# Kernel optimization log

Hardware: AMD Instinct MI355X
Metric: run time of the kernel (lower is better)

The kernel has to match this reference:

```python
import jax, jax.numpy as jnp
import numpy as np

N_QUBITS = 11   # state dim 2**11 = 2048
N_LAYERS = 6
BATCH = 8192


def _rz(phi):
    # RZ(phi) = diag(e^{-i phi/2}, e^{+i phi/2}); phi scalar -> (2,2), phi (B,) -> (B,2,2)
    e = jnp.exp(-0.5j * phi.astype(jnp.complex64))
    z = jnp.zeros_like(e)
    return jnp.stack([jnp.stack([e, z], -1), jnp.stack([z, jnp.conj(e)], -1)], -2)


def _ry(theta):
    # RY(theta) = [[cos t, -sin t], [sin t, cos t]], t = theta/2
    t = 0.5 * theta.astype(jnp.float32)
    c = jnp.cos(t).astype(jnp.complex64)
    s = jnp.sin(t).astype(jnp.complex64)
    return jnp.stack([jnp.stack([c, -s], -1), jnp.stack([s, c], -1)], -2)


def _apply_1q(state, U, q, n):
    # state: (B, 2**n); qubit q is the q-th most-significant bit of the ket index
    B = state.shape[0]
    st = state.reshape(B, 2 ** q, 2, 2 ** (n - 1 - q))
    if U.ndim == 2:   # shared (trainable) gate
        st = jnp.einsum('ab,sxby->sxay', U, st)
    else:             # per-sample (data-encoding) gate, U: (B,2,2)
        st = jnp.einsum('sab,sxby->sxay', U, st)
    return st.reshape(B, 2 ** n)


def _apply_cnot(state, c, n):
    # CNOT with control c, target c+1 (adjacent in the chain)
    B = state.shape[0]
    st = state.reshape(B, 2 ** c, 2, 2, 2 ** (n - 2 - c))
    st = jnp.stack([st[:, :, 0], st[:, :, 1, ::-1]], axis=2)  # flip target when control=1
    return st.reshape(B, 2 ** n)


def _forward(X, params):
    n, L = N_QUBITS, N_LAYERS
    B = X.shape[0]
    # pad/truncate features to n_qubits (matches build_circuit)
    Xe = X[:, :n] if X.shape[1] >= n else jnp.pad(X, ((0, 0), (0, n - X.shape[1])))
    state = jnp.zeros((B, 2 ** n), jnp.complex64).at[:, 0].set(1.0)  # |0...0>
    for l in range(L):
        for q in range(n):
            state = _apply_1q(state, _rz(params[l, q, 0]), q, n)
            state = _apply_1q(state, _ry(params[l, q, 1]), q, n)
            state = _apply_1q(state, _rz(params[l, q, 2]), q, n)
            if l == L - 1:  # data re-upload RY only on the last layer (per source)
                state = _apply_1q(state, _ry(Xe[:, q]), q, n)
        if n > 1:
            for c in range(n - 1):
                state = _apply_cnot(state, c, n)
    return state  # (B, 2**n) complex64


def setup_inputs() -> dict:
    key = jax.random.key(0)
    k1, k2 = jax.random.split(key)
    X = jax.random.uniform(k1, (BATCH, N_QUBITS), jnp.float32) * (2.0 * np.pi)
    params = jax.random.normal(k2, (N_LAYERS, N_QUBITS, 3), jnp.float32) * 0.01
    return {"X": X, "params": params}


def reference(X, params):
    state = _forward(X, params)
    # return real/imag stacked so the output is a real float32 array
    return jnp.stack([state.real, state.imag], -1)  # (B, 2**n, 2)
```

## Files before the change

### kernel.cpp

```cpp
#include <hip/hip_runtime.h>
#include <math.h>

#define NQ   11
#define DIM  2048
#define NL   6

typedef float v2f __attribute__((ext_vector_type(2)));

__host__ __device__ constexpr int swzA(int x) {
    return x ^ ((x >> 6) & 31) ^ ((x & 2) << 3) ^ ((x & 1) << 3);
}
__host__ __device__ constexpr int swzB(int x) {
    return x ^ ((x >> 7) & 7) ^ ((x >> 3) & 14) ^ ((x >> 6) & 8);
}

__device__ __forceinline__ float2 cfma2(float2 u, float2 a, float2 v, float2 b) {
    float2 r;
    r.x = u.x*a.x - u.y*a.y + v.x*b.x - v.y*b.y;
    r.y = u.x*a.y + u.y*a.x + v.x*b.y + v.y*b.x;
    return r;
}

template<int CTRL>
__device__ __forceinline__ v2f dpp_xor(v2f v) {
    const int x = __builtin_amdgcn_update_dpp(
        0, __float_as_int(v.x), CTRL, 0xF, 0xF, true);
    const int y = __builtin_amdgcn_update_dpp(
        0, __float_as_int(v.y), CTRL, 0xF, 0xF, true);
    v2f r; r.x = __int_as_float(x); r.y = __int_as_float(y);
    return r;
}

__global__ __launch_bounds__(256) void qnn_shared_kernel(
    const float* __restrict__ P,
    float2* __restrict__ ws)
{
    __shared__ float2 lds[DIM];
    __shared__ float2 G[NL*NQ][4];
    const int t = threadIdx.x;

    if (t < NL*NQ) {
        const float p0 = P[t*3+0], p1 = P[t*3+1], p2 = P[t*3+2];
        const float th = 0.5f*p1;
        const float c  = cosf(th), s = sinf(th);
        const float al = 0.5f*(p0+p2), be = 0.5f*(p0-p2);
        const float ca = cosf(al), sa = sinf(al);
        const float cb = cosf(be), sb = sinf(be);
        G[t][0] = make_float2( c*ca, -c*sa);
        G[t][1] = make_float2(-s*cb, -s*sb);
        G[t][2] = make_float2( s*cb, -s*sb);
        G[t][3] = make_float2( c*ca,  c*sa);
    }

    const int a0w = swzA(t);
    const int a1b = swzA(((t>>5)<<8) | (t&31));
    const int a2b = swzA(((t>>2)<<5) | (t&3));
    const int a3b = swzA(t ^ (t>>1));
    const int natb = ((t>>2)<<5) | (t&3);

    float2 a[8];
    #pragma unroll
    for (int k = 0; k < 8; ++k) a[k] = make_float2(0.f, 0.f);
    if (t == 0) a[0] = make_float2(1.f, 0.f);
    __syncthreads();

    #define CG(g_, rb_) { \
        const float2 U00=G[g_][0], U01=G[g_][1], U10=G[g_][2], U11=G[g_][3]; \
        _Pragma("unroll") \
        for (int kk = 0; kk < 8; ++kk) if (!(kk & (rb_))) { \
            const float2 a0 = a[kk], a1 = a[kk|(rb_)]; \
            a[kk]       = cfma2(U00, a0, U01, a1); \
            a[kk|(rb_)] = cfma2(U10, a0, U11, a1); \
        } }

    #define SG(g_, m_, b_) { \
        const float2 ca_ = (b_) ? G[g_][3] : G[g_][0]; \
        const float2 cb_ = (b_) ? G[g_][2] : G[g_][1]; \
        _Pragma("unroll") \
        for (int kk = 0; kk < 8; ++kk) { \
            float2 p; \
            p.x = __shfl_xor(a[kk].x, m_); \
            p.y = __shfl_xor(a[kk].y, m_); \
            a[kk] = cfma2(ca_, a[kk], cb_, p); \
        } }

    for (int l = 0; l < NL; ++l) {
        const int g0 = l*NQ;
        CG(g0+0, 4) CG(g0+1, 2) CG(g0+2, 1)

        #pragma unroll
        for (int k = 0; k < 8; ++k) lds[a0w ^ swzA(k<<8)] = a[k];
        __syncthreads();
        #pragma unroll
        for (int k = 0; k < 8; ++k) a[k] = lds[a1b ^ swzA(k<<5)];
        __syncthreads();
        CG(g0+3, 4) CG(g0+4, 2) CG(g0+5, 1)

        #pragma unroll
        for (int k = 0; k < 8; ++k) lds[a1b ^ swzA(k<<5)] = a[k];
        __syncthreads();
        #pragma unroll
        for (int k = 0; k < 8; ++k) a[k] = lds[a2b ^ swzA(k<<2)];
        __syncthreads();
        CG(g0+6, 4) CG(g0+7, 2) CG(g0+8, 1)

        SG(g0+9, 2, (t>>1)&1)
        SG(g0+10, 1, t&1)

        if (l < NL-1) {
            #pragma unroll
            for (int k = 0; k < 8; ++k) lds[a2b ^ swzA(k<<2)] = a[k];
            __syncthreads();
            #pragma unroll
            for (int k = 0; k < 8; ++k)
                a[k] = lds[a3b ^ swzA((k<<8) ^ (k<<7))];
            __syncthreads();
        } else {
            #pragma unroll
            for (int k = 0; k < 8; ++k) ws[natb | (k<<2)] = a[k];
        }
    }
    #undef CG
    #undef SG
}

__global__ __launch_bounds__(128, 4) void qnn_last_kernel(
    const float* __restrict__ X,
    const float2* __restrict__ S5,
    float2* __restrict__ out)
{
    __shared__ float2 lds[DIM];
    __shared__ float2 gc[NQ];
    const int b = blockIdx.x;
    const int t = threadIdx.x;

    if (t < NQ) {
        const float tx = 0.5f * X[(size_t)b*NQ + t];
        gc[t] = make_float2(cosf(tx), sinf(tx));
    }

    const int b0 = swzB(t);
    const int b1 = swzB(((t>>3)<<7) | (t&7));
    const int b3 = swzB(t ^ (t>>1));

    v2f a[16];
    #pragma unroll
    for (int k = 0; k < 16; ++k) {
        const float2 v = S5[(k<<7) | t];
        a[k] = (v2f){v.x, v.y};
    }
    __syncthreads();

    #define RG(q_, rb_) { \
        const float c = gc[q_].x, s = gc[q_].y; \
        _Pragma("unroll") \
        for (int kk = 0; kk < 16; ++kk) if (!(kk & (rb_))) { \
            const v2f a0 = a[kk], a1 = a[kk|(rb_)]; \
            a[kk]       = c*a0 - s*a1; \
            a[kk|(rb_)] = s*a0 + c*a1; \
        } }

    #define LGD(q_, CTRL_, r_) { \
        const float c = gc[q_].x, s = gc[q_].y; \
        const float sg = (r_) ? s : -s; \
        _Pragma("unroll") \
        for (int kk = 0; kk < 16; ++kk) { \
            const v2f p = dpp_xor<CTRL_>(a[kk]); \
            a[kk] = c*a[kk] + sg*p; \
        } }

    RG(0, 8) RG(1, 4) RG(2, 2) RG(3, 1)

    #pragma unroll
    for (int k = 0; k < 16; ++k)
        lds[b0 ^ swzB(k<<7)] = make_float2(a[k].x, a[k].y);
    __syncthreads();
    #pragma unroll
    for (int k = 0; k < 16; ++k) {
        const float2 v = lds[b1 ^ swzB(k<<3)];
        a[k] = (v2f){v.x, v.y};
    }
    RG(4, 8) RG(5, 4) RG(6, 2) RG(7, 1)

    #pragma unroll
    for (int k = 0; k < 16; ++k)
        lds[b1 ^ swzB(k<<3)] = make_float2(a[k].x, a[k].y);
    __syncthreads();
    #pragma unroll
    for (int k = 0; k < 16; ++k) {
        const float2 v = lds[b3 ^ swzB((k<<7) ^ (k<<6))];
        a[k] = (v2f){v.x, v.y};
    }

    LGD(8, 0x141, ((t>>2) ^ (t>>3)) & 1)
    LGD(9, 27,    ((t>>1) ^ (t>>2)) & 1)
    LGD(10, 177,  ( t     ^ (t>>1)) & 1)

    float2* o = out + (size_t)b * DIM + t;
    #pragma unroll
    for (int k = 0; k < 16; ++k)
        o[k<<7] = make_float2(a[k].x, a[k].y);
    #undef RG
    #undef LGD
}

extern "C" void kernel_launch(void* const* d_in, const int* in_sizes, int n_in,
                              void* d_out, int out_size, void* d_ws, size_t ws_size,
                              hipStream_t stream) {
    const float* X = (const float*)d_in[0];
    const float* P = (const float*)d_in[1];
    float2* out = (float2*)d_out;
    float2* ws  = (float2*)d_ws;
    const int B = in_sizes[0] / NQ;
    qnn_shared_kernel<<<1, 256, 0, stream>>>(P, ws);
    qnn_last_kernel<<<B, 128, 0, stream>>>(X, ws, out);
}
```

Measured before the change: 52.46 us.

## Process several samples per block reusing shared state, vectorize complex math, trim barriers

The per-sample kernel now handles four samples per block and loads the shared pre-layer state from global memory once per block, reusing it across those samples. This cuts redundant global reads and block launch overhead. It also uses lighter LDS barriers (waitcnt plus s_barrier) and removes some barriers after LDS reads in the single-block kernel. Complex multiplies are rewritten as packed two-wide vector FMAs. The trade-off is fewer blocks (2048), each running a serial loop, which may reduce latency hiding and adds register pressure from keeping both m[16] and a[16] live.

```diff
diff --git a/kernel.cpp b/kernel.cpp
--- a/kernel.cpp
+++ b/kernel.cpp
@@ -4,6 +4,7 @@
 #define NQ   11
 #define DIM  2048
 #define NL   6
+#define SPB  4
 
 typedef float v2f __attribute__((ext_vector_type(2)));
 
@@ -14,12 +15,10 @@
     return x ^ ((x >> 7) & 7) ^ ((x >> 3) & 14) ^ ((x >> 6) & 8);
 }
 
-__device__ __forceinline__ float2 cfma2(float2 u, float2 a, float2 v, float2 b) {
-    float2 r;
-    r.x = u.x*a.x - u.y*a.y + v.x*b.x - v.y*b.y;
-    r.y = u.x*a.y + u.y*a.x + v.x*b.y + v.y*b.x;
-    return r;
-}
+#define BAR_LDS() do { \
+    asm volatile("s_waitcnt lgkmcnt(0)" ::: "memory"); \
+    __builtin_amdgcn_s_barrier(); \
+} while (0)
 
 template<int CTRL>
 __device__ __forceinline__ v2f dpp_xor(v2f v) {
@@ -31,12 +30,22 @@
     return r;
 }
 
+__device__ __forceinline__ void cpair(const v2f U00, const v2f U01,
+                                      const v2f U10, const v2f U11,
+                                      v2f& A0, v2f& A1) {
+    const v2f a0 = A0, a1 = A1;
+    const v2f a0i = {-a0.y, a0.x};
+    const v2f a1i = {-a1.y, a1.x};
+    A0 = U00.x*a0 + U00.y*a0i + U01.x*a1 + U01.y*a1i;
+    A1 = U10.x*a0 + U10.y*a0i + U11.x*a1 + U11.y*a1i;
+}
+
 __global__ __launch_bounds__(256) void qnn_shared_kernel(
     const float* __restrict__ P,
     float2* __restrict__ ws)
 {
-    __shared__ float2 lds[DIM];
-    __shared__ float2 G[NL*NQ][4];
+    __shared__ v2f lds[DIM];
+    __shared__ v2f G[NL*NQ][4];
     const int t = threadIdx.x;
 
     if (t < NL*NQ) {
@@ -46,10 +55,10 @@
         const float al = 0.5f*(p0+p2), be = 0.5f*(p0-p2);
         const float ca = cosf(al), sa = sinf(al);
         const float cb = cosf(be), sb = sinf(be);
-        G[t][0] = make_float2( c*ca, -c*sa);
-        G[t][1] = make_float2(-s*cb, -s*sb);
-        G[t][2] = make_float2( s*cb, -s*sb);
-        G[t][3] = make_float2( c*ca,  c*sa);
+        G[t][0] = (v2f){ c*ca, -c*sa};
+        G[t][1] = (v2f){-s*cb, -s*sb};
+        G[t][2] = (v2f){ s*cb, -s*sb};
+        G[t][3] = (v2f){ c*ca,  c*sa};
     }
 
     const int a0w = swzA(t);
@@ -58,30 +67,30 @@
     const int a3b = swzA(t ^ (t>>1));
     const int natb = ((t>>2)<<5) | (t&3);
 
-    float2 a[8];
+    v2f a[8];
     #pragma unroll
-    for (int k = 0; k < 8; ++k) a[k] = make_float2(0.f, 0.f);
-    if (t == 0) a[0] = make_float2(1.f, 0.f);
+    for (int k = 0; k < 8; ++k) a[k] = (v2f){0.f, 0.f};
+    if (t == 0) a[0] = (v2f){1.f, 0.f};
     __syncthreads();
 
     #define CG(g_, rb_) { \
-        const float2 U00=G[g_][0], U01=G[g_][1], U10=G[g_][2], U11=G[g_][3]; \
-        _Pragma("unroll") \
-        for (int kk = 0; kk < 8; ++kk) if (!(kk & (rb_))) { \
-            const float2 a0 = a[kk], a1 = a[kk|(rb_)]; \
-            a[kk]       = cfma2(U00, a0, U01, a1); \
-            a[kk|(rb_)] = cfma2(U10, a0, U11, a1); \
-        } }
+        const v2f U00=G[g_][0], U01=G[g_][1], U10=G[g_][2], U11=G[g_][3]; \
+        _Pragma("unroll") \
+        for (int kk = 0; kk < 8; ++kk) if (!(kk & (rb_))) \
+            cpair(U00, U01, U10, U11, a[kk], a[kk|(rb_)]); \
+    }
 
     #define SG(g_, m_, b_) { \
-        const float2 ca_ = (b_) ? G[g_][3] : G[g_][0]; \
-        const float2 cb_ = (b_) ? G[g_][2] : G[g_][1]; \
+        const v2f ca_ = (b_) ? G[g_][3] : G[g_][0]; \
+        const v2f cb_ = (b_) ? G[g_][2] : G[g_][1]; \
         _Pragma("unroll") \
         for (int kk = 0; kk < 8; ++kk) { \
-            float2 p; \
+            v2f p; \
             p.x = __shfl_xor(a[kk].x, m_); \
             p.y = __shfl_xor(a[kk].y, m_); \
-            a[kk] = cfma2(ca_, a[kk], cb_, p); \
+            const v2f si = {-a[kk].y, a[kk].x}; \
+            const v2f pi = {-p.y, p.x}; \
+            a[kk] = ca_.x*a[kk] + ca_.y*si + cb_.x*p + cb_.y*pi; \
         } }
 
     for (int l = 0; l < NL; ++l) {
@@ -93,7 +102,6 @@
         __syncthreads();
         #pragma unroll
         for (int k = 0; k < 8; ++k) a[k] = lds[a1b ^ swzA(k<<5)];
-        __syncthreads();
         CG(g0+3, 4) CG(g0+4, 2) CG(g0+5, 1)
 
         #pragma unroll
@@ -101,7 +109,6 @@
         __syncthreads();
         #pragma unroll
         for (int k = 0; k < 8; ++k) a[k] = lds[a2b ^ swzA(k<<2)];
-        __syncthreads();
         CG(g0+6, 4) CG(g0+7, 2) CG(g0+8, 1)
 
         SG(g0+9, 2, (t>>1)&1)
@@ -117,7 +124,8 @@
             __syncthreads();
         } else {
             #pragma unroll
-            for (int k = 0; k < 8; ++k) ws[natb | (k<<2)] = a[k];
+            for (int k = 0; k < 8; ++k)
+                ws[natb | (k<<2)] = make_float2(a[k].x, a[k].y);
         }
     }
     #undef CG
@@ -127,79 +135,95 @@
 __global__ __launch_bounds__(128, 4) void qnn_last_kernel(
     const float* __restrict__ X,
     const float2* __restrict__ S5,
-    float2* __restrict__ out)
+    float2* __restrict__ out,
+    const int B)
 {
     __shared__ float2 lds[DIM];
-    __shared__ float2 gc[NQ];
-    const int b = blockIdx.x;
-    const int t = threadIdx.x;
-
-    if (t < NQ) {
-        const float tx = 0.5f * X[(size_t)b*NQ + t];
-        gc[t] = make_float2(cosf(tx), sinf(tx));
-    }
-
-    const int b0 = swzB(t);
-    const int b1 = swzB(((t>>3)<<7) | (t&7));
-    const int b3 = swzB(t ^ (t>>1));
-
-    v2f a[16];
+    __shared__ float2 gcs[SPB][NQ];
+    const int t  = threadIdx.x;
+    const int b0 = blockIdx.x * SPB;
+    const int ns = min(SPB, B - b0);
+
+    if (t < ns*NQ) {
+        const int si = t / NQ, q = t - si*NQ;
+        const float tx = 0.5f * X[(size_t)(b0+si)*NQ + q];
+        gcs[si][q] = make_float2(cosf(tx), sinf(tx));
+    }
+
+    const int w0 = swzB(t);
+    const int w1 = swzB(((t>>3)<<7) | (t&7));
+    const int w3 = swzB(t ^ (t>>1));
+
+    v2f m[16];
     #pragma unroll
     for (int k = 0; k < 16; ++k) {
         const float2 v = S5[(k<<7) | t];
-        a[k] = (v2f){v.x, v.y};
+        m[k] = (v2f){v.x, v.y};
     }
     __syncthreads();
 
     #define RG(q_, rb_) { \
-        const float c = gc[q_].x, s = gc[q_].y; \
+        const float c = gcs[s][q_].x, sn = gcs[s][q_].y; \
         _Pragma("unroll") \
         for (int kk = 0; kk < 16; ++kk) if (!(kk & (rb_))) { \
             const v2f a0 = a[kk], a1 = a[kk|(rb_)]; \
-            a[kk]       = c*a0 - s*a1; \
-            a[kk|(rb_)] = s*a0 + c*a1; \
+            a[kk]       = c*a0 - sn*a1; \
+            a[kk|(rb_)] = sn*a0 + c*a1; \
         } }
 
     #define LGD(q_, CTRL_, r_) { \
-        const float c = gc[q_].x, s = gc[q_].y; \
-        const float sg = (r_) ? s : -s; \
+        const float c = gcs[s][q_].x, sn = gcs[s][q_].y; \
+        const float sg = (r_) ? sn : -sn; \
         _Pragma("unroll") \
         for (int kk = 0; kk < 16; ++kk) { \
             const v2f p = dpp_xor<CTRL_>(a[kk]); \
             a[kk] = c*a[kk] + sg*p; \
         } }
 
-    RG(0, 8) RG(1, 4) RG(2, 2) RG(3, 1)
-
-    #pragma unroll
-    for (int k = 0; k < 16; ++k)
-        lds[b0 ^ swzB(k<<7)] = make_float2(a[k].x, a[k].y);
-    __syncthreads();
-    #pragma unroll
-    for (int k = 0; k < 16; ++k) {
-        const float2 v = lds[b1 ^ swzB(k<<3)];
-        a[k] = (v2f){v.x, v.y};
-    }
-    RG(4, 8) RG(5, 4) RG(6, 2) RG(7, 1)
-
-    #pragma unroll
-    for (int k = 0; k < 16; ++k)
-        lds[b1 ^ swzB(k<<3)] = make_float2(a[k].x, a[k].y);
-    __syncthreads();
-    #pragma unroll
-    for (int k = 0; k < 16; ++k) {
-        const float2 v = lds[b3 ^ swzB((k<<7) ^ (k<<6))];
-        a[k] = (v2f){v.x, v.y};
-    }
-
-    LGD(8, 0x141, ((t>>2) ^ (t>>3)) & 1)
-    LGD(9, 27,    ((t>>1) ^ (t>>2)) & 1)
-    LGD(10, 177,  ( t     ^ (t>>1)) & 1)
-
-    float2* o = out + (size_t)b * DIM + t;
-    #pragma unroll
-    for (int k = 0; k < 16; ++k)
-        o[k<<7] = make_float2(a[k].x, a[k].y);
+    for (int s = 0; s < ns; ++s) {
+        v2f a[16];
+        {
+            const float c = gcs[s][0].x, sn = gcs[s][0].y;
+            #pragma unroll
+            for (int kk = 0; kk < 8; ++kk) {
+                a[kk]   = c*m[kk] - sn*m[kk|8];
+                a[kk|8] = sn*m[kk] + c*m[kk|8];
+            }
+        }
+        RG(1, 4) RG(2, 2) RG(3, 1)
+
+        #pragma unroll
+        for (int k = 0; k < 16; ++k)
+            lds[w0 ^ swzB(k<<7)] = make_float2(a[k].x, a[k].y);
+        BAR_LDS();
+        #pragma unroll
+        for (int k = 0; k < 16; ++k) {
+            const float2 v = lds[w1 ^ swzB(k<<3)];
+            a[k] = (v2f){v.x, v.y};
+        }
+        RG(4, 8) RG(5, 4) RG(6, 2) RG(7, 1)
+
+        #pragma unroll
+        for (int k = 0; k < 16; ++k)
+            lds[w1 ^ swzB(k<<3)] = make_float2(a[k].x, a[k].y);
+        BAR_LDS();
+        #pragma unroll
+        for (int k = 0; k < 16; ++k) {
+            const float2 v = lds[w3 ^ swzB((k<<7) ^ (k<<6))];
+            a[k] = (v2f){v.x, v.y};
+        }
+
+        LGD(8, 0x141, ((t>>2) ^ (t>>3)) & 1)
+        LGD(9, 27,    ((t>>1) ^ (t>>2)) & 1)
+        LGD(10, 177,  ( t     ^ (t>>1)) & 1)
+
+        float2* o = out + (size_t)(b0+s) * DIM + t;
+        #pragma unroll
+        for (int k = 0; k < 16; ++k)
+            o[k<<7] = make_float2(a[k].x, a[k].y);
+
+        BAR_LDS();
+    }
     #undef RG
     #undef LGD
 }
@@ -212,6 +236,7 @@
     float2* out = (float2*)d_out;
     float2* ws  = (float2*)d_ws;
     const int B = in_sizes[0] / NQ;
+    const int nb = (B + SPB - 1) / SPB;
     qnn_shared_kernel<<<1, 256, 0, stream>>>(P, ws);
-    qnn_last_kernel<<<B, 128, 0, stream>>>(X, ws, out);
-}
+    qnn_last_kernel<<<nb, 128, 0, stream>>>(X, ws, out, B);
+}
```

Measured after the change: 62.61 us. 1.19x slower.

## Use float4 pair-wide loads/stores and remap qubit stages in last-layer kernel

Applied to the files above, without the earlier changes.

Reworks the per-sample last-layer kernel so each thread holds adjacent amplitude pairs (the least-significant qubit kept in-register). Global loads, global stores and LDS traffic become float4 instead of float2. The qubit-to-register mapping is reorganized: qubit 10 is applied first in registers, and a Gray-code style permutation (hperm) is used for the final LDS transpose so the CNOT-chain-affected qubits can be handled with DPP lane exchanges. The aim is fewer, wider memory transactions on the output-bound write. The risk is LDS bank conflicts from the unswizzled float4 layout and subtle correctness issues in the new permutation.

```diff
diff --git a/kernel.cpp b/kernel.cpp
--- a/kernel.cpp
+++ b/kernel.cpp
@@ -10,8 +10,9 @@
 __host__ __device__ constexpr int swzA(int x) {
     return x ^ ((x >> 6) & 31) ^ ((x & 2) << 3) ^ ((x & 1) << 3);
 }
-__host__ __device__ constexpr int swzB(int x) {
-    return x ^ ((x >> 7) & 7) ^ ((x >> 3) & 14) ^ ((x >> 6) & 8);
+__host__ __device__ constexpr int hperm(int x) {
+    return x ^ (x>>1) ^ (x>>2) ^ (x>>3) ^ (x>>4) ^ (x>>5)
+             ^ (x>>6) ^ (x>>7) ^ (x>>8) ^ (x>>9) ^ (x>>10);
 }
 
 __device__ __forceinline__ float2 cfma2(float2 u, float2 a, float2 v, float2 b) {
@@ -126,10 +127,10 @@
 
 __global__ __launch_bounds__(128, 4) void qnn_last_kernel(
     const float* __restrict__ X,
-    const float2* __restrict__ S5,
-    float2* __restrict__ out)
+    const float4* __restrict__ S5c,
+    float4* __restrict__ out4)
 {
-    __shared__ float2 lds[DIM];
+    __shared__ float4 ldsc[DIM/2];
     __shared__ float2 gc[NQ];
     const int b = blockIdx.x;
     const int t = threadIdx.x;
@@ -139,69 +140,87 @@
         gc[t] = make_float2(cosf(tx), sinf(tx));
     }
 
-    const int b0 = swzB(t);
-    const int b1 = swzB(((t>>3)<<7) | (t&7));
-    const int b3 = swzB(t ^ (t>>1));
-
     v2f a[16];
     #pragma unroll
-    for (int k = 0; k < 16; ++k) {
-        const float2 v = S5[(k<<7) | t];
-        a[k] = (v2f){v.x, v.y};
+    for (int k = 0; k < 8; ++k) {
+        const float4 v = S5c[(k<<7) | t];
+        a[2*k]   = (v2f){v.x, v.y};
+        a[2*k+1] = (v2f){v.z, v.w};
     }
     __syncthreads();
 
     #define RG(q_, rb_) { \
-        const float c = gc[q_].x, s = gc[q_].y; \
-        _Pragma("unroll") \
-        for (int kk = 0; kk < 16; ++kk) if (!(kk & (rb_))) { \
-            const v2f a0 = a[kk], a1 = a[kk|(rb_)]; \
-            a[kk]       = c*a0 - s*a1; \
-            a[kk|(rb_)] = s*a0 + c*a1; \
-        } }
-
-    #define LGD(q_, CTRL_, r_) { \
-        const float c = gc[q_].x, s = gc[q_].y; \
-        const float sg = (r_) ? s : -s; \
-        _Pragma("unroll") \
-        for (int kk = 0; kk < 16; ++kk) { \
-            const v2f p = dpp_xor<CTRL_>(a[kk]); \
-            a[kk] = c*a[kk] + sg*p; \
-        } }
-
-    RG(0, 8) RG(1, 4) RG(2, 2) RG(3, 1)
-
-    #pragma unroll
-    for (int k = 0; k < 16; ++k)
-        lds[b0 ^ swzB(k<<7)] = make_float2(a[k].x, a[k].y);
-    __syncthreads();
-    #pragma unroll
-    for (int k = 0; k < 16; ++k) {
-        const float2 v = lds[b1 ^ swzB(k<<3)];
-        a[k] = (v2f){v.x, v.y};
-    }
-    RG(4, 8) RG(5, 4) RG(6, 2) RG(7, 1)
-
-    #pragma unroll
-    for (int k = 0; k < 16; ++k)
-        lds[b1 ^ swzB(k<<3)] = make_float2(a[k].x, a[k].y);
-    __syncthreads();
-    #pragma unroll
-    for (int k = 0; k < 16; ++k) {
-        const float2 v = lds[b3 ^ swzB((k<<7) ^ (k<<6))];
-        a[k] = (v2f){v.x, v.y};
-    }
-
-    LGD(8, 0x141, ((t>>2) ^ (t>>3)) & 1)
-    LGD(9, 27,    ((t>>1) ^ (t>>2)) & 1)
-    LGD(10, 177,  ( t     ^ (t>>1)) & 1)
-
-    float2* o = out + (size_t)b * DIM + t;
-    #pragma unroll
-    for (int k = 0; k < 16; ++k)
-        o[k<<7] = make_float2(a[k].x, a[k].y);
+        const float c = gc[q_].x, sn = gc[q_].y; \
+        const v2f cc = {c, c}, sv = {sn, sn}; \
+        _Pragma("unroll") \
+        for (int j = 0; j < 16; ++j) if (!(j & (rb_))) { \
+            const v2f a0 = a[j], a1 = a[j|(rb_)]; \
+            a[j]       = cc*a0 - sv*a1; \
+            a[j|(rb_)] = sv*a0 + cc*a1; \
+        } }
+
+    #define CGD(q_, CTRL_, r_) { \
+        const float c = gc[q_].x, sn = gc[q_].y; \
+        const float sg = (r_) ? sn : -sn; \
+        const v2f cc = {c, c}, sgv = {sg, sg}; \
+        _Pragma("unroll") \
+        for (int k = 0; k < 8; ++k) { \
+            const v2f o0 = a[2*k], o1 = a[2*k+1]; \
+            const v2f p0 = dpp_xor<CTRL_>(o1); \
+            const v2f p1 = dpp_xor<CTRL_>(o0); \
+            a[2*k]   = cc*o0 + sgv*p0; \
+            a[2*k+1] = cc*o1 + sgv*p1; \
+        } }
+
+    RG(0, 8) RG(1, 4) RG(2, 2) RG(10, 1)
+
+    #pragma unroll
+    for (int k = 0; k < 8; ++k)
+        ldsc[(k<<7) | t] = make_float4(a[2*k].x, a[2*k].y, a[2*k+1].x, a[2*k+1].y);
+    __syncthreads();
+    const int cR = ((t>>4)<<7) | (t & 15);
+    #pragma unroll
+    for (int k = 0; k < 8; ++k) {
+        const float4 v = ldsc[cR | (k<<4)];
+        a[2*k]   = (v2f){v.x, v.y};
+        a[2*k+1] = (v2f){v.z, v.w};
+    }
+    RG(3, 8) RG(4, 4) RG(5, 2)
+    __syncthreads();
+
+    {
+        const int sB    = (((t>>4)&7)<<8) | (((t>>1)&7)<<2) | ((t&1)<<1);
+        const int cellB = hperm(sB) >> 1;
+        const int pt    = __popc(t) & 1;
+        #pragma unroll
+        for (int k = 0; k < 8; ++k) {
+            const int cell = cellB ^ (hperm(k<<5) >> 1);
+            const bool sw  = (pt ^ (__popc(k) & 1)) != 0;
+            const v2f lo = sw ? a[2*k+1] : a[2*k];
+            const v2f hi = sw ? a[2*k]   : a[2*k+1];
+            ldsc[cell] = make_float4(lo.x, lo.y, hi.x, hi.y);
+        }
+    }
+    __syncthreads();
+
+    #pragma unroll
+    for (int k = 0; k < 8; ++k) {
+        const float4 v = ldsc[(k<<7) | t];
+        a[2*k]   = (v2f){v.x, v.y};
+        a[2*k+1] = (v2f){v.z, v.w};
+    }
+
+    CGD(6, 0x140, ((t>>3) ^ (t>>4)) & 1)
+    CGD(7, 0x141, ((t>>2) ^ (t>>3)) & 1)
+    CGD(8, 27,    ((t>>1) ^ (t>>2)) & 1)
+    CGD(9, 177,   ( t     ^ (t>>1)) & 1)
+
+    float4* o = out4 + (size_t)b * (DIM/2);
+    #pragma unroll
+    for (int k = 0; k < 8; ++k)
+        o[(k<<7) | t] = make_float4(a[2*k].x, a[2*k].y, a[2*k+1].x, a[2*k+1].y);
     #undef RG
-    #undef LGD
+    #undef CGD
 }
 
 extern "C" void kernel_launch(void* const* d_in, const int* in_sizes, int n_in,
@@ -209,9 +228,8 @@
                               hipStream_t stream) {
     const float* X = (const float*)d_in[0];
     const float* P = (const float*)d_in[1];
-    float2* out = (float2*)d_out;
     float2* ws  = (float2*)d_ws;
     const int B = in_sizes[0] / NQ;
     qnn_shared_kernel<<<1, 256, 0, stream>>>(P, ws);
-    qnn_last_kernel<<<B, 128, 0, stream>>>(X, ws, out);
-}
+    qnn_last_kernel<<<B, 128, 0, stream>>>(X, (const float4*)ws, (float4*)d_out);
+}
```

Result: no change. 52.12 us (-0.6%).
